# Performance work log

Hardware: AMD Instinct MI355X
Metric: run time of the kernel (lower is better)

## Reference

```python
import jax, jax.numpy as jnp
import numpy as np

MARGIN = 0.3  # hinge margin (init kwarg)


def setup_inputs() -> dict:
    key = jax.random.key(0)
    k1, k2 = jax.random.split(key)
    B, D, C = 384, 256, 24
    e = jax.random.normal(k1, (B, D), dtype=jnp.float32)
    e = e / jnp.linalg.norm(e, axis=1, keepdims=True)  # module expects L2-normalized embeddings
    labels = jax.random.randint(k2, (B,), 0, C)
    return {"embeddings": e, "labels": labels}


def reference(embeddings, labels):
    B = embeddings.shape[0]
    # squared pairwise euclidean distances (== torch.cdist(...).pow(2))
    sq = jnp.sum(embeddings * embeddings, axis=1)
    dist = jnp.maximum(sq[:, None] + sq[None, :] - 2.0 * (embeddings @ embeddings.T), 0.0)  # [B,B]

    eq = labels[:, None] == labels[None, :]
    eye = jnp.eye(B, dtype=bool)
    pos_mask = eq & ~eye            # valid (anchor, positive) pairs
    neg_mask = ~eq                  # valid (anchor, negative) pairs

    INF = jnp.float32(np.inf)
    d_ap = dist                      # [B,B]: d(anchor i, positive p)
    d_n = dist[:, None, :]           # [B,1,B]: d(anchor i, negative n)

    # semi-hard: negatives farther than the positive but within margin  -> [B,B,B]
    semi = neg_mask[:, None, :] & (d_n > d_ap[:, :, None]) & (d_n < d_ap[:, :, None] + MARGIN)
    d_semi = jnp.min(jnp.where(semi, d_n, INF), axis=-1)   # [B,B]
    has_semi = jnp.any(semi, axis=-1)                      # [B,B]

    # fallback: hardest (closest) negative per anchor
    d_negmin = jnp.min(jnp.where(neg_mask, dist, INF), axis=-1)  # [B]
    d_an = jnp.where(has_semi, d_semi, d_negmin[:, None])        # [B,B]

    has_neg = jnp.any(neg_mask, axis=1)                    # [B]
    valid = pos_mask & has_neg[:, None]                    # triplets actually counted

    losses = jnp.maximum(d_ap - d_an + MARGIN, 0.0)
    num_valid = jnp.maximum(jnp.sum(valid), 1).astype(jnp.float32)
    return jnp.sum(jnp.where(valid, losses, 0.0)) / num_valid
```

## Files before the change

### kernel.cpp

```cpp
#include <hip/hip_runtime.h>
#include <math.h>

#define NB 384
#define ND4 64
#define NW 6
#define NC 32
#define TMARGIN 0.3f

__global__ __launch_bounds__(NB) void triplet_fused(
    const float4* __restrict__ E4, const int* __restrict__ labels,
    float* __restrict__ out)
{
    const int a = blockIdx.x;
    const int t = threadIdx.x;
    const int w = t >> 6;
    const int l = t & 63;
    const int s = l & 7;
    const int g = l >> 3;

    __shared__ float4 sa4[ND4];
    __shared__ float  sdist[NB];
    __shared__ int    slabel[NB];
    __shared__ int    spos[NB];
    __shared__ int    shist[NC];
    __shared__ int    scount;
    __shared__ float  swred[NW];
    __shared__ float  snegmin;

    if (t == 0) scount = 0;
    if (t < NC) shist[t] = 0;
    if (t < ND4) sa4[t] = E4[a * ND4 + t];
    const int lt = labels[t];
    slabel[t] = lt;
    __syncthreads();
    atomicAdd(&shist[lt], 1);

    float4 u[8];
    #pragma unroll
    for (int j = 0; j < 8; ++j) u[j] = sa4[s + (j << 3)];

    #pragma unroll
    for (int i = 0; i < 8; ++i) {
        const int row = (w << 6) + (i << 3) + g;
        const float4* __restrict__ p = E4 + row * ND4 + s;
        float d = 0.f;
        #pragma unroll
        for (int j = 0; j < 8; ++j) {
            float4 v = p[j << 3];
            float dx = v.x - u[j].x, dy = v.y - u[j].y;
            float dz = v.z - u[j].z, dq = v.w - u[j].w;
            d += dx*dx + dy*dy + dz*dz + dq*dq;
        }
        d += __shfl_xor(d, 1, 64);
        d += __shfl_xor(d, 2, 64);
        d += __shfl_xor(d, 4, 64);
        if (s == 0) sdist[row] = d;
    }
    __syncthreads();

    const int la = slabel[a];

    float nm = (slabel[t] != la) ? sdist[t] : INFINITY;
    #pragma unroll
    for (int off = 32; off > 0; off >>= 1)
        nm = fminf(nm, __shfl_xor(nm, off, 64));
    if (l == 0) swred[w] = nm;
    if (slabel[t] == la && t != a) {
        int idx = atomicAdd(&scount, 1);
        spos[idx] = t;
    }
    __syncthreads();
    if (t == 0) {
        float m = swred[0];
        #pragma unroll
        for (int i = 1; i < NW; ++i) m = fminf(m, swred[i]);
        snegmin = m;
    }
    __syncthreads();

    const float negmin  = snegmin;
    const int   P       = scount;
    const bool  has_neg = (negmin < INFINITY);

    float lsum = 0.f;
    if (has_neg) {
        for (int pi = w; pi < P; pi += NW) {
            const int   p  = spos[pi];
            const float dp = sdist[p];
            const float hi = dp + TMARGIN;
            float m = INFINITY;
            #pragma unroll
            for (int i = 0; i < NB / 64; ++i) {
                const int   n  = (i << 6) + l;
                const float dn = sdist[n];
                if ((slabel[n] != la) && (dn > dp) && (dn < hi))
                    m = fminf(m, dn);
            }
            #pragma unroll
            for (int off = 32; off > 0; off >>= 1)
                m = fminf(m, __shfl_xor(m, off, 64));
            if (l == 0) {
                const float dan = (m < INFINITY) ? m : negmin;
                lsum += fmaxf(dp - dan + TMARGIN, 0.f);
            }
        }
    }

    __syncthreads();
    if (l == 0) swred[w] = lsum;
    __syncthreads();
    if (t == 0) {
        float ssum = swred[0];
        #pragma unroll
        for (int i = 1; i < NW; ++i) ssum += swred[i];
        if (ssum != 0.f) {
            int nv = 0;
            #pragma unroll
            for (int c = 0; c < NC; ++c) {
                const int n = shist[c];
                if (n < NB) nv += n * (n - 1);
            }
            atomicAdd(out, ssum / (float)(nv > 0 ? nv : 1));
        }
    }
}

extern "C" void kernel_launch(void* const* d_in, const int* in_sizes, int n_in,
                              void* d_out, int out_size, void* d_ws, size_t ws_size,
                              hipStream_t stream) {
    (void)in_sizes; (void)n_in; (void)d_ws; (void)ws_size; (void)out_size;
    const float4* emb  = (const float4*)d_in[0];
    const int* labels  = (const int*)d_in[1];

    float* out = (float*)d_out;
    hipMemsetAsync(out, 0, sizeof(float), stream);
    triplet_fused<<<NB, NB, 0, stream>>>(emb, labels, out);
}
```

Measured before the change: 68.74 us.

## Process two anchors per block, sharing embedding row loads via dot-product distances

Each block now handles two anchor rows, so every streamed embedding row is reused for two distances. The distance is rewritten from a direct squared difference to |a|^2 + |v|^2 - 2a·v, which allows the shared row load. The semi-hard search loop interleaves positives from both anchors across warps. This halves the grid to 192 blocks, which reduces global loads but lowers parallelism on a GPU with many CUs. It also raises per-thread register use through the two anchor vectors.

Result: faster. 66.89 us (-2.7%).

```diff
diff --git a/kernel.cpp b/kernel.cpp
--- a/kernel.cpp
+++ b/kernel.cpp
@@ -5,114 +5,142 @@
 #define ND4 64
 #define NW 6
 #define NC 32
+#define NA 2
+#define NBLK (NB/NA)
 #define TMARGIN 0.3f
 
 __global__ __launch_bounds__(NB) void triplet_fused(
     const float4* __restrict__ E4, const int* __restrict__ labels,
     float* __restrict__ out)
 {
-    const int a = blockIdx.x;
+    const int a0 = blockIdx.x * NA;
     const int t = threadIdx.x;
     const int w = t >> 6;
     const int l = t & 63;
     const int s = l & 7;
     const int g = l >> 3;
 
-    __shared__ float4 sa4[ND4];
-    __shared__ float  sdist[NB];
+    __shared__ float4 sa4[NA][ND4];
+    __shared__ float  sdist[NA][NB];
     __shared__ int    slabel[NB];
-    __shared__ int    spos[NB];
+    __shared__ int    spos[NA][NB];
     __shared__ int    shist[NC];
-    __shared__ int    scount;
-    __shared__ float  swred[NW];
-    __shared__ float  snegmin;
+    __shared__ int    scount[NA];
+    __shared__ float  swred[NA][NW];
+    __shared__ float  snegmin[NA];
 
-    if (t == 0) scount = 0;
+    if (t < NA) scount[t] = 0;
     if (t < NC) shist[t] = 0;
-    if (t < ND4) sa4[t] = E4[a * ND4 + t];
+    if (t < NA * ND4) ((float4*)sa4)[t] = E4[a0 * ND4 + t];
     const int lt = labels[t];
     slabel[t] = lt;
     __syncthreads();
     atomicAdd(&shist[lt], 1);
 
-    float4 u[8];
+    float4 u0[8], u1[8];
     #pragma unroll
-    for (int j = 0; j < 8; ++j) u[j] = sa4[s + (j << 3)];
+    for (int j = 0; j < 8; ++j) {
+        u0[j] = sa4[0][s + (j << 3)];
+        u1[j] = sa4[1][s + (j << 3)];
+    }
+
+    float sqa0 = 0.f, sqa1 = 0.f;
+    #pragma unroll
+    for (int j = 0; j < 8; ++j) {
+        sqa0 += u0[j].x*u0[j].x + u0[j].y*u0[j].y + u0[j].z*u0[j].z + u0[j].w*u0[j].w;
+        sqa1 += u1[j].x*u1[j].x + u1[j].y*u1[j].y + u1[j].z*u1[j].z + u1[j].w*u1[j].w;
+    }
+    #pragma unroll
+    for (int off = 1; off < 8; off <<= 1) {
+        sqa0 += __shfl_xor(sqa0, off, 64);
+        sqa1 += __shfl_xor(sqa1, off, 64);
+    }
 
     #pragma unroll
     for (int i = 0; i < 8; ++i) {
         const int row = (w << 6) + (i << 3) + g;
         const float4* __restrict__ p = E4 + row * ND4 + s;
-        float d = 0.f;
+        float dot0 = 0.f, dot1 = 0.f, sqv = 0.f;
         #pragma unroll
         for (int j = 0; j < 8; ++j) {
             float4 v = p[j << 3];
-            float dx = v.x - u[j].x, dy = v.y - u[j].y;
-            float dz = v.z - u[j].z, dq = v.w - u[j].w;
-            d += dx*dx + dy*dy + dz*dz + dq*dq;
+            dot0 += v.x*u0[j].x + v.y*u0[j].y + v.z*u0[j].z + v.w*u0[j].w;
+            dot1 += v.x*u1[j].x + v.y*u1[j].y + v.z*u1[j].z + v.w*u1[j].w;
+            sqv  += v.x*v.x + v.y*v.y + v.z*v.z + v.w*v.w;
         }
-        d += __shfl_xor(d, 1, 64);
-        d += __shfl_xor(d, 2, 64);
-        d += __shfl_xor(d, 4, 64);
-        if (s == 0) sdist[row] = d;
+        #pragma unroll
+        for (int off = 1; off < 8; off <<= 1) {
+            dot0 += __shfl_xor(dot0, off, 64);
+            dot1 += __shfl_xor(dot1, off, 64);
+            sqv  += __shfl_xor(sqv , off, 64);
+        }
+        if (s == 0) {
+            sdist[0][row] = fmaxf(sqv + sqa0 - 2.f * dot0, 0.f);
+            sdist[1][row] = fmaxf(sqv + sqa1 - 2.f * dot1, 0.f);
+        }
     }
     __syncthreads();
 
-    const int la = slabel[a];
+    const int la0 = slabel[a0];
+    const int la1 = slabel[a0 + 1];
 
-    float nm = (slabel[t] != la) ? sdist[t] : INFINITY;
+    float nm0 = (lt != la0) ? sdist[0][t] : INFINITY;
+    float nm1 = (lt != la1) ? sdist[1][t] : INFINITY;
     #pragma unroll
-    for (int off = 32; off > 0; off >>= 1)
-        nm = fminf(nm, __shfl_xor(nm, off, 64));
-    if (l == 0) swred[w] = nm;
-    if (slabel[t] == la && t != a) {
-        int idx = atomicAdd(&scount, 1);
-        spos[idx] = t;
+    for (int off = 32; off > 0; off >>= 1) {
+        nm0 = fminf(nm0, __shfl_xor(nm0, off, 64));
+        nm1 = fminf(nm1, __shfl_xor(nm1, off, 64));
     }
+    if (l == 0) { swred[0][w] = nm0; swred[1][w] = nm1; }
+    if (lt == la0 && t != a0)     spos[0][atomicAdd(&scount[0], 1)] = t;
+    if (lt == la1 && t != a0 + 1) spos[1][atomicAdd(&scount[1], 1)] = t;
     __syncthreads();
-    if (t == 0) {
-        float m = swred[0];
+    if (t < NA) {
+        float m = swred[t][0];
         #pragma unroll
-        for (int i = 1; i < NW; ++i) m = fminf(m, swred[i]);
-        snegmin = m;
+        for (int i = 1; i < NW; ++i) m = fminf(m, swred[t][i]);
+        snegmin[t] = m;
     }
     __syncthreads();
 
-    const float negmin  = snegmin;
-    const int   P       = scount;
-    const bool  has_neg = (negmin < INFINITY);
+    const float ng0 = snegmin[0], ng1 = snegmin[1];
+    const int   P0  = scount[0],  P1  = scount[1];
 
     float lsum = 0.f;
-    if (has_neg) {
-        for (int pi = w; pi < P; pi += NW) {
-            const int   p  = spos[pi];
-            const float dp = sdist[p];
-            const float hi = dp + TMARGIN;
-            float m = INFINITY;
-            #pragma unroll
-            for (int i = 0; i < NB / 64; ++i) {
-                const int   n  = (i << 6) + l;
-                const float dn = sdist[n];
-                if ((slabel[n] != la) && (dn > dp) && (dn < hi))
-                    m = fminf(m, dn);
-            }
-            #pragma unroll
-            for (int off = 32; off > 0; off >>= 1)
-                m = fminf(m, __shfl_xor(m, off, 64));
-            if (l == 0) {
-                const float dan = (m < INFINITY) ? m : negmin;
-                lsum += fmaxf(dp - dan + TMARGIN, 0.f);
-            }
+    const int total = P0 + P1;
+    for (int pi = w; pi < total; pi += NW) {
+        const int   which = (pi >= P0) ? 1 : 0;
+        const float nmW   = which ? ng1 : ng0;
+        if (nmW == INFINITY) continue;
+        const int   la  = which ? la1 : la0;
+        const float* __restrict__ dst = sdist[which];
+        const int   p   = spos[which][which ? pi - P0 : pi];
+        const float dp  = dst[p];
+        const float hi  = dp + TMARGIN;
+        float m = INFINITY;
+        #pragma unroll
+        for (int i = 0; i < NB / 64; ++i) {
+            const int   n  = (i << 6) + l;
+            const float dn = dst[n];
+            if ((slabel[n] != la) && (dn > dp) && (dn < hi))
+                m = fminf(m, dn);
+        }
+        #pragma unroll
+        for (int off = 32; off > 0; off >>= 1)
+            m = fminf(m, __shfl_xor(m, off, 64));
+        if (l == 0) {
+            const float dan = (m < INFINITY) ? m : nmW;
+            lsum += fmaxf(dp - dan + TMARGIN, 0.f);
         }
     }
 
     __syncthreads();
-    if (l == 0) swred[w] = lsum;
+    if (l == 0) swred[0][w] = lsum;
     __syncthreads();
     if (t == 0) {
-        float ssum = swred[0];
+        float ssum = swred[0][0];
         #pragma unroll
-        for (int i = 1; i < NW; ++i) ssum += swred[i];
+        for (int i = 1; i < NW; ++i) ssum += swred[0][i];
         if (ssum != 0.f) {
             int nv = 0;
             #pragma unroll
@@ -134,5 +162,5 @@
 
     float* out = (float*)d_out;
     hipMemsetAsync(out, 0, sizeof(float), stream);
-    triplet_fused<<<NB, NB, 0, stream>>>(emb, labels, out);
+    triplet_fused<<<NBLK, NB, 0, stream>>>(emb, labels, out);
 }
```
